# Performance work log

Measured on AMD Instinct MI355X. Metric: run time of the kernel, lower is better.

Reference implementation:

```python
import jax, jax.numpy as jnp
import numpy as np

WINDOW_SIZE = 11
SIGMA = 1.5
C1 = 0.01 ** 2
C2 = 0.03 ** 2


def _gaussian_window(window_size: int, channel: int) -> jnp.ndarray:
    # 1D gaussian, normalized
    g = jnp.arange(window_size, dtype=jnp.float32) - window_size // 2
    g = jnp.exp(-(g ** 2) / (2.0 * SIGMA ** 2))
    g = g / g.sum()
    w2d = jnp.outer(g, g)  # [K, K]
    # depthwise conv kernel: [C, 1, K, K] in OIHW with feature_group_count=C
    return jnp.broadcast_to(w2d[None, None], (channel, 1, window_size, window_size))


def _depthwise_conv(x: jnp.ndarray, window: jnp.ndarray, channel: int) -> jnp.ndarray:
    pad = WINDOW_SIZE // 2
    return jax.lax.conv_general_dilated(
        x, window,
        window_strides=(1, 1),
        padding=((pad, pad), (pad, pad)),
        dimension_numbers=('NCHW', 'OIHW', 'NCHW'),
        feature_group_count=channel,
    )


def setup_inputs() -> dict:
    key = jax.random.key(0)
    k1, k2 = jax.random.split(key)
    shape = (16, 3, 512, 512)
    img1 = jax.random.uniform(k1, shape, dtype=jnp.float32)
    img2 = jax.random.uniform(k2, shape, dtype=jnp.float32)
    return {"img1": img1, "img2": img2}


def reference(img1, img2):
    channel = img1.shape[1]
    window = _gaussian_window(WINDOW_SIZE, channel).astype(img1.dtype)

    mu1 = _depthwise_conv(img1, window, channel)
    mu2 = _depthwise_conv(img2, window, channel)

    mu1_sq = mu1 * mu1
    mu2_sq = mu2 * mu2
    mu1_mu2 = mu1 * mu2

    sigma1_sq = _depthwise_conv(img1 * img1, window, channel) - mu1_sq
    sigma2_sq = _depthwise_conv(img2 * img2, window, channel) - mu2_sq
    sigma12 = _depthwise_conv(img1 * img2, window, channel) - mu1_mu2

    ssim_map = ((2.0 * mu1_mu2 + C1) * (2.0 * sigma12 + C2)) / (
        (mu1_sq + mu2_sq + C1) * (sigma1_sq + sigma2_sq + C2))

    return 1.0 - ssim_map.mean()
```

## Files before the change

### kernel.cpp

```cpp
#include <hip/hip_runtime.h>

#define IMG_W 512
#define IMG_H 512
#define PLANE_PX (IMG_W * IMG_H)
#define N_ELEMS (48 * PLANE_PX)
#define NTHREADS 256
#define TILEW 48
#define NCT 11
#define NBANDS 8
#define NBLK (48 * NBANDS * NCT)

#define C1x2 2.0e-4f
#define C2x2 1.8e-3f

typedef _Float16 h2 __attribute__((ext_vector_type(2)));
typedef _Float16 h8 __attribute__((ext_vector_type(8)));
typedef float f32x4 __attribute__((ext_vector_type(4)));
typedef __fp16 fp16v2 __attribute__((ext_vector_type(2)));

__device__ __forceinline__ h2 h2fma(_Float16 w, h2 v, h2 acc) {
    h2 wv = {w, w};
    return __builtin_elementwise_fma(wv, v, acc);
}
__device__ __forceinline__ unsigned int h2bits(h2 v) {
    union { h2 h; unsigned int u; } c; c.h = v; return c.u;
}
__device__ __forceinline__ h2 pkrtz(float x, float y) {
    union { fp16v2 f; h2 h; } c;
    c.f = __builtin_amdgcn_cvt_pkrtz(x, y);
    return c.h;
}

__global__ void __launch_bounds__(NTHREADS, 5) ssim_main(
    const float* __restrict__ img1, const float* __restrict__ img2,
    float* __restrict__ partials)
{
    __shared__ __align__(16) uint2 R[64 * 64];

    constexpr _Float16 Gh[11] = {
        (_Float16)0.00102838f, (_Float16)0.00759876f, (_Float16)0.03600077f,
        (_Float16)0.10936070f, (_Float16)0.21300553f, (_Float16)0.26601173f,
        (_Float16)0.21300553f, (_Float16)0.10936070f, (_Float16)0.03600077f,
        (_Float16)0.00759876f, (_Float16)0.00102838f
    };

    const int tid = threadIdx.x;

    const int xcd = blockIdx.x & 7;
    const int idx = blockIdx.x >> 3;
    const int plane = xcd * 6 + idx / 88;
    const int t = idx % 88;
    const int band = t / 11;
    const int ct = t - band * 11;
    const int tx0 = ct * TILEW;
    const int ty0 = band * 64;
    const float* pa = img1 + (size_t)plane * PLANE_PX;
    const float* pb = img2 + (size_t)plane * PLANE_PX;

    const int c = tid & 63;
    const int g = tid >> 6;
    const int gx = tx0 - 5 + c;
    const int cgx = min(max(gx, 0), IMG_W - 1);
    const int ry0 = ty0 + g * 16 - 5;

    float av[26], bv[26];
    const bool intY = (ry0 >= 0) && (ry0 + 26 <= IMG_H);
    if (intY) {
        const float* qa = pa + (size_t)ry0 * IMG_W + cgx;
        const float* qb = pb + (size_t)ry0 * IMG_W + cgx;
#pragma unroll
        for (int j = 0; j < 26; ++j) {
            av[j] = qa[j * IMG_W];
            bv[j] = qb[j * IMG_W];
        }
    } else {
#pragma unroll
        for (int j = 0; j < 26; ++j) {
            int ry = ry0 + j;
            int ryc = min(max(ry, 0), IMG_H - 1);
            float rm = ((unsigned)ry < (unsigned)IMG_H) ? 1.f : 0.f;
            av[j] = pa[(size_t)ryc * IMG_W + cgx] * rm;
            bv[j] = pb[(size_t)ryc * IMG_W + cgx] * rm;
        }
    }

    h2 asd[16], asq[16];
#pragma unroll
    for (int k = 0; k < 16; ++k) { asd[k] = (h2)(_Float16)0; asq[k] = (h2)(_Float16)0; }
#pragma unroll
    for (int j = 0; j < 26; ++j) {
        h2 sd = pkrtz(av[j] + bv[j], av[j] - bv[j]);
        h2 sq = sd * sd;
#pragma unroll
        for (int k = 0; k < 16; ++k) {
            int tt = j - k;
            if (tt >= 0 && tt < 11) {
                asd[k] = h2fma(Gh[tt], sd, asd[k]);
                asq[k] = h2fma(Gh[tt], sq, asq[k]);
            }
        }
    }

    if (ct == 0 || ct == NCT - 1) {
        const _Float16 ml = ((unsigned)gx < (unsigned)IMG_W) ? (_Float16)1.f
                                                             : (_Float16)0.f;
        const h2 mlv = {ml, ml};
#pragma unroll
        for (int k = 0; k < 16; ++k) { asd[k] = asd[k] * mlv; asq[k] = asq[k] * mlv; }
    }
#pragma unroll
    for (int kk = 0; kk < 16; ++kk) {
        const int row = g * 16 + kk;
        const int sc = c ^ ((kk & 7) << 1);
        R[row * 64 + sc] = make_uint2(h2bits(asd[kk]), h2bits(asq[kk]));
    }
    __syncthreads();

    const int lane = tid & 63;
    const int nrow = lane & 15;
    const int khi = lane >> 4;
    const int rs = tid >> 6;
    const int row_lds = rs * 16 + nrow;
    const int swz = (nrow & 7) << 1;
    const uint2* Rrow = R + row_lds * 64;

    int sidx = min(lane, 10 - lane);
    unsigned gvb = 0u;
    gvb = (sidx == 0) ? 0x1436u : gvb;
    gvb = (sidx == 1) ? 0x1FC8u : gvb;
    gvb = (sidx == 2) ? 0x289Cu : gvb;
    gvb = (sidx == 3) ? 0x2F00u : gvb;
    gvb = (sidx == 4) ? 0x32D1u : gvb;
    gvb = (sidx == 5) ? 0x3442u : gvb;
    union { h8 h; unsigned u[4]; } af;
#pragma unroll
    for (int w = 0; w < 4; ++w) {
        int t0 = khi * 8 + 2 * w - nrow;
        unsigned lo = (unsigned)__shfl((int)gvb, t0 & 63, 64);
        unsigned hi = (unsigned)__shfl((int)gvb, (t0 + 1) & 63, 64);
        af.u[w] = (lo & 0xFFFFu) | (hi << 16);
    }

    float local = 0.f;
#pragma unroll
    for (int mg = 0; mg < 3; ++mg) {
        if (tx0 + mg * 16 < IMG_W) {
            const int cb = mg * 16 + khi * 8;
            const uint4 q0 = *(const uint4*)&Rrow[(cb + 0) ^ swz];
            const uint4 q1 = *(const uint4*)&Rrow[(cb + 2) ^ swz];
            const uint4 q2 = *(const uint4*)&Rrow[(cb + 4) ^ swz];
            const uint4 q3 = *(const uint4*)&Rrow[(cb + 6) ^ swz];

            union { h8 h; unsigned u[4]; } fs, fd, fss, fdd;
            fs.u[0]  = (q0.x & 0xFFFFu) | (q0.z << 16);
            fs.u[1]  = (q1.x & 0xFFFFu) | (q1.z << 16);
            fs.u[2]  = (q2.x & 0xFFFFu) | (q2.z << 16);
            fs.u[3]  = (q3.x & 0xFFFFu) | (q3.z << 16);
            fd.u[0]  = (q0.x >> 16) | (q0.z & 0xFFFF0000u);
            fd.u[1]  = (q1.x >> 16) | (q1.z & 0xFFFF0000u);
            fd.u[2]  = (q2.x >> 16) | (q2.z & 0xFFFF0000u);
            fd.u[3]  = (q3.x >> 16) | (q3.z & 0xFFFF0000u);
            fss.u[0] = (q0.y & 0xFFFFu) | (q0.w << 16);
            fss.u[1] = (q1.y & 0xFFFFu) | (q1.w << 16);
            fss.u[2] = (q2.y & 0xFFFFu) | (q2.w << 16);
            fss.u[3] = (q3.y & 0xFFFFu) | (q3.w << 16);
            fdd.u[0] = (q0.y >> 16) | (q0.w & 0xFFFF0000u);
            fdd.u[1] = (q1.y >> 16) | (q1.w & 0xFFFF0000u);
            fdd.u[2] = (q2.y >> 16) | (q2.w & 0xFFFF0000u);
            fdd.u[3] = (q3.y >> 16) | (q3.w & 0xFFFF0000u);

            const f32x4 z = {0.f, 0.f, 0.f, 0.f};
            f32x4 aS  = __builtin_amdgcn_mfma_f32_16x16x32_f16(af.h, fs.h,  z, 0, 0, 0);
            f32x4 aD  = __builtin_amdgcn_mfma_f32_16x16x32_f16(af.h, fd.h,  z, 0, 0, 0);
            f32x4 aSS = __builtin_amdgcn_mfma_f32_16x16x32_f16(af.h, fss.h, z, 0, 0, 0);
            f32x4 aDD = __builtin_amdgcn_mfma_f32_16x16x32_f16(af.h, fdd.h, z, 0, 0, 0);

#pragma unroll
            for (int i = 0; i < 4; ++i) {
                float cs = aS[i], cd = aD[i], css = aSS[i], cdd = aDD[i];
                float P = cs * cs, Q = cd * cd;
                float U = P - Q;
                float V = P + Q;
                float num = (U + C1x2) * ((css - cdd) - U + C2x2);
                float den = (V + C1x2) * ((css + cdd) - V + C2x2);
                local += num * __builtin_amdgcn_rcpf(den);
            }
        }
    }

#pragma unroll
    for (int off = 32; off > 0; off >>= 1) local += __shfl_down(local, off, 64);
    __syncthreads();
    float* wp = (float*)R;
    if (lane == 0) wp[rs] = local;
    __syncthreads();
    if (tid == 0)
        partials[blockIdx.x] = wp[0] + wp[1] + wp[2] + wp[3];
}

__global__ void ssim_final(const float* __restrict__ partials,
                           float* __restrict__ out)
{
    __shared__ float wp[4];
    const int tid = threadIdx.x;
    const float4* p4 = (const float4*)partials;
    float s = 0.f;
    for (int i = tid; i < NBLK / 4; i += NTHREADS) {
        float4 v = p4[i];
        s += (v.x + v.y) + (v.z + v.w);
    }
#pragma unroll
    for (int off = 32; off > 0; off >>= 1) s += __shfl_down(s, off, 64);
    if ((tid & 63) == 0) wp[tid >> 6] = s;
    __syncthreads();
    if (tid == 0)
        out[0] = 1.0f - (wp[0] + wp[1] + wp[2] + wp[3]) * (1.0f / (float)N_ELEMS);
}

extern "C" void kernel_launch(void* const* d_in, const int* in_sizes, int n_in,
                              void* d_out, int out_size, void* d_ws, size_t ws_size,
                              hipStream_t stream) {
    const float* img1 = (const float*)d_in[0];
    const float* img2 = (const float*)d_in[1];
    float* out = (float*)d_out;
    float* partials = (float*)d_ws;

    ssim_main<<<NBLK, NTHREADS, 0, stream>>>(img1, img2, partials);
    ssim_final<<<1, NTHREADS, 0, stream>>>(partials, out);
}
```

Before: 127.8 us.

## Move vertical Gaussian pass onto MFMA and store per-quantity planes in LDS

The vertical 11-tap convolution, previously done with scalar packed-half FMAs over 26 register rows per thread, now runs as MFMA 16x16x32 matrix multiplies against a banded Gaussian matrix. Each wave loads 8 rows per lane for 4 column chunks. The results for S, D, SS and DD go into four separate swizzled LDS planes, so the horizontal pass can read each operand with a single 16-byte load and skips the bit-unpacking shuffle. This removes most of the VALU FMA work and the large register arrays, but it adds redundant global loads from overlapping rows and a second fp16 rounding of the intermediate results.

```diff
diff --git a/kernel.cpp b/kernel.cpp
--- a/kernel.cpp
+++ b/kernel.cpp
@@ -18,10 +18,6 @@
 typedef float f32x4 __attribute__((ext_vector_type(4)));
 typedef __fp16 fp16v2 __attribute__((ext_vector_type(2)));
 
-__device__ __forceinline__ h2 h2fma(_Float16 w, h2 v, h2 acc) {
-    h2 wv = {w, w};
-    return __builtin_elementwise_fma(wv, v, acc);
-}
 __device__ __forceinline__ unsigned int h2bits(h2 v) {
     union { h2 h; unsigned int u; } c; c.h = v; return c.u;
 }
@@ -35,94 +31,24 @@
     const float* __restrict__ img1, const float* __restrict__ img2,
     float* __restrict__ partials)
 {
-    __shared__ __align__(16) uint2 R[64 * 64];
-
-    constexpr _Float16 Gh[11] = {
-        (_Float16)0.00102838f, (_Float16)0.00759876f, (_Float16)0.03600077f,
-        (_Float16)0.10936070f, (_Float16)0.21300553f, (_Float16)0.26601173f,
-        (_Float16)0.21300553f, (_Float16)0.10936070f, (_Float16)0.03600077f,
-        (_Float16)0.00759876f, (_Float16)0.00102838f
-    };
+    __shared__ __align__(16) unsigned short P[4 * 64 * 64];
 
     const int tid = threadIdx.x;
+    const int lane = tid & 63;
+    const int wv = tid >> 6;
+    const int nr = lane & 15;
+    const int khi = lane >> 4;
 
     const int xcd = blockIdx.x & 7;
     const int idx = blockIdx.x >> 3;
-    const int plane = xcd * 6 + idx / 88;
+    const int pl = xcd * 6 + idx / 88;
     const int t = idx % 88;
     const int band = t / 11;
     const int ct = t - band * 11;
     const int tx0 = ct * TILEW;
     const int ty0 = band * 64;
-    const float* pa = img1 + (size_t)plane * PLANE_PX;
-    const float* pb = img2 + (size_t)plane * PLANE_PX;
-
-    const int c = tid & 63;
-    const int g = tid >> 6;
-    const int gx = tx0 - 5 + c;
-    const int cgx = min(max(gx, 0), IMG_W - 1);
-    const int ry0 = ty0 + g * 16 - 5;
-
-    float av[26], bv[26];
-    const bool intY = (ry0 >= 0) && (ry0 + 26 <= IMG_H);
-    if (intY) {
-        const float* qa = pa + (size_t)ry0 * IMG_W + cgx;
-        const float* qb = pb + (size_t)ry0 * IMG_W + cgx;
-#pragma unroll
-        for (int j = 0; j < 26; ++j) {
-            av[j] = qa[j * IMG_W];
-            bv[j] = qb[j * IMG_W];
-        }
-    } else {
-#pragma unroll
-        for (int j = 0; j < 26; ++j) {
-            int ry = ry0 + j;
-            int ryc = min(max(ry, 0), IMG_H - 1);
-            float rm = ((unsigned)ry < (unsigned)IMG_H) ? 1.f : 0.f;
-            av[j] = pa[(size_t)ryc * IMG_W + cgx] * rm;
-            bv[j] = pb[(size_t)ryc * IMG_W + cgx] * rm;
-        }
-    }
-
-    h2 asd[16], asq[16];
-#pragma unroll
-    for (int k = 0; k < 16; ++k) { asd[k] = (h2)(_Float16)0; asq[k] = (h2)(_Float16)0; }
-#pragma unroll
-    for (int j = 0; j < 26; ++j) {
-        h2 sd = pkrtz(av[j] + bv[j], av[j] - bv[j]);
-        h2 sq = sd * sd;
-#pragma unroll
-        for (int k = 0; k < 16; ++k) {
-            int tt = j - k;
-            if (tt >= 0 && tt < 11) {
-                asd[k] = h2fma(Gh[tt], sd, asd[k]);
-                asq[k] = h2fma(Gh[tt], sq, asq[k]);
-            }
-        }
-    }
-
-    if (ct == 0 || ct == NCT - 1) {
-        const _Float16 ml = ((unsigned)gx < (unsigned)IMG_W) ? (_Float16)1.f
-                                                             : (_Float16)0.f;
-        const h2 mlv = {ml, ml};
-#pragma unroll
-        for (int k = 0; k < 16; ++k) { asd[k] = asd[k] * mlv; asq[k] = asq[k] * mlv; }
-    }
-#pragma unroll
-    for (int kk = 0; kk < 16; ++kk) {
-        const int row = g * 16 + kk;
-        const int sc = c ^ ((kk & 7) << 1);
-        R[row * 64 + sc] = make_uint2(h2bits(asd[kk]), h2bits(asq[kk]));
-    }
-    __syncthreads();
-
-    const int lane = tid & 63;
-    const int nrow = lane & 15;
-    const int khi = lane >> 4;
-    const int rs = tid >> 6;
-    const int row_lds = rs * 16 + nrow;
-    const int swz = (nrow & 7) << 1;
-    const uint2* Rrow = R + row_lds * 64;
+    const float* pa = img1 + (size_t)pl * PLANE_PX;
+    const float* pb = img2 + (size_t)pl * PLANE_PX;
 
     int sidx = min(lane, 10 - lane);
     unsigned gvb = 0u;
@@ -135,52 +61,102 @@
     union { h8 h; unsigned u[4]; } af;
 #pragma unroll
     for (int w = 0; w < 4; ++w) {
-        int t0 = khi * 8 + 2 * w - nrow;
+        int t0 = khi * 8 + 2 * w - nr;
         unsigned lo = (unsigned)__shfl((int)gvb, t0 & 63, 64);
         unsigned hi = (unsigned)__shfl((int)gvb, (t0 + 1) & 63, 64);
         af.u[w] = (lo & 0xFFFFu) | (hi << 16);
     }
 
+    const f32x4 z = {0.f, 0.f, 0.f, 0.f};
+
+    const int ry0 = ty0 + wv * 16 - 5;
+    const int ryb = ry0 + khi * 8;
+    const bool fastY = (ry0 >= 0) && (ry0 + 31 < IMG_H);
+    const bool edge = (ct == 0) || (ct == NCT - 1);
+
+#pragma unroll
+    for (int tc = 0; tc < 4; ++tc) {
+        const int gx = tx0 - 5 + tc * 16 + nr;
+        const int cgx = min(max(gx, 0), IMG_W - 1);
+        float s[8], d[8];
+        if (fastY) {
+            const float* qa = pa + (size_t)ryb * IMG_W + cgx;
+            const float* qb = pb + (size_t)ryb * IMG_W + cgx;
+#pragma unroll
+            for (int j = 0; j < 8; ++j) {
+                float a = qa[j * IMG_W], b = qb[j * IMG_W];
+                s[j] = a + b; d[j] = a - b;
+            }
+        } else {
+#pragma unroll
+            for (int j = 0; j < 8; ++j) {
+                int ry = ryb + j;
+                int ryc = min(max(ry, 0), IMG_H - 1);
+                float rm = ((unsigned)ry < (unsigned)IMG_H) ? 1.f : 0.f;
+                float a = pa[(size_t)ryc * IMG_W + cgx] * rm;
+                float b = pb[(size_t)ryc * IMG_W + cgx] * rm;
+                s[j] = a + b; d[j] = a - b;
+            }
+        }
+        union { h8 h; h2 p[4]; } FS, FD, FSS, FDD;
+#pragma unroll
+        for (int w = 0; w < 4; ++w) {
+            FS.p[w] = pkrtz(s[2 * w], s[2 * w + 1]);
+            FD.p[w] = pkrtz(d[2 * w], d[2 * w + 1]);
+        }
+        if (edge) {
+            const _Float16 ml = ((unsigned)gx < (unsigned)IMG_W) ? (_Float16)1.f
+                                                                 : (_Float16)0.f;
+            const h2 mlv = {ml, ml};
+#pragma unroll
+            for (int w = 0; w < 4; ++w) { FS.p[w] *= mlv; FD.p[w] *= mlv; }
+        }
+#pragma unroll
+        for (int w = 0; w < 4; ++w) {
+            FSS.p[w] = FS.p[w] * FS.p[w];
+            FDD.p[w] = FD.p[w] * FD.p[w];
+        }
+        f32x4 oS  = __builtin_amdgcn_mfma_f32_16x16x32_f16(FS.h,  af.h, z, 0, 0, 0);
+        f32x4 oD  = __builtin_amdgcn_mfma_f32_16x16x32_f16(FD.h,  af.h, z, 0, 0, 0);
+        f32x4 oSS = __builtin_amdgcn_mfma_f32_16x16x32_f16(FSS.h, af.h, z, 0, 0, 0);
+        f32x4 oDD = __builtin_amdgcn_mfma_f32_16x16x32_f16(FDD.h, af.h, z, 0, 0, 0);
+
+        const int prow = wv * 16 + nr;
+        const int swc = (tc * 16 + khi * 4) ^ ((nr & 7) << 3);
+        unsigned short* q = &P[prow * 64 + swc];
+        *(uint2*)(q)         = make_uint2(h2bits(pkrtz(oS[0],  oS[1])),
+                                          h2bits(pkrtz(oS[2],  oS[3])));
+        *(uint2*)(q + 4096)  = make_uint2(h2bits(pkrtz(oD[0],  oD[1])),
+                                          h2bits(pkrtz(oD[2],  oD[3])));
+        *(uint2*)(q + 8192)  = make_uint2(h2bits(pkrtz(oSS[0], oSS[1])),
+                                          h2bits(pkrtz(oSS[2], oSS[3])));
+        *(uint2*)(q + 12288) = make_uint2(h2bits(pkrtz(oDD[0], oDD[1])),
+                                          h2bits(pkrtz(oDD[2], oDD[3])));
+    }
+    __syncthreads();
+
+    const int row = wv * 16 + nr;
     float local = 0.f;
 #pragma unroll
     for (int mg = 0; mg < 3; ++mg) {
         if (tx0 + mg * 16 < IMG_W) {
-            const int cb = mg * 16 + khi * 8;
-            const uint4 q0 = *(const uint4*)&Rrow[(cb + 0) ^ swz];
-            const uint4 q1 = *(const uint4*)&Rrow[(cb + 2) ^ swz];
-            const uint4 q2 = *(const uint4*)&Rrow[(cb + 4) ^ swz];
-            const uint4 q3 = *(const uint4*)&Rrow[(cb + 6) ^ swz];
-
-            union { h8 h; unsigned u[4]; } fs, fd, fss, fdd;
-            fs.u[0]  = (q0.x & 0xFFFFu) | (q0.z << 16);
-            fs.u[1]  = (q1.x & 0xFFFFu) | (q1.z << 16);
-            fs.u[2]  = (q2.x & 0xFFFFu) | (q2.z << 16);
-            fs.u[3]  = (q3.x & 0xFFFFu) | (q3.z << 16);
-            fd.u[0]  = (q0.x >> 16) | (q0.z & 0xFFFF0000u);
-            fd.u[1]  = (q1.x >> 16) | (q1.z & 0xFFFF0000u);
-            fd.u[2]  = (q2.x >> 16) | (q2.z & 0xFFFF0000u);
-            fd.u[3]  = (q3.x >> 16) | (q3.z & 0xFFFF0000u);
-            fss.u[0] = (q0.y & 0xFFFFu) | (q0.w << 16);
-            fss.u[1] = (q1.y & 0xFFFFu) | (q1.w << 16);
-            fss.u[2] = (q2.y & 0xFFFFu) | (q2.w << 16);
-            fss.u[3] = (q3.y & 0xFFFFu) | (q3.w << 16);
-            fdd.u[0] = (q0.y >> 16) | (q0.w & 0xFFFF0000u);
-            fdd.u[1] = (q1.y >> 16) | (q1.w & 0xFFFF0000u);
-            fdd.u[2] = (q2.y >> 16) | (q2.w & 0xFFFF0000u);
-            fdd.u[3] = (q3.y >> 16) | (q3.w & 0xFFFF0000u);
-
-            const f32x4 z = {0.f, 0.f, 0.f, 0.f};
-            f32x4 aS  = __builtin_amdgcn_mfma_f32_16x16x32_f16(af.h, fs.h,  z, 0, 0, 0);
-            f32x4 aD  = __builtin_amdgcn_mfma_f32_16x16x32_f16(af.h, fd.h,  z, 0, 0, 0);
-            f32x4 aSS = __builtin_amdgcn_mfma_f32_16x16x32_f16(af.h, fss.h, z, 0, 0, 0);
-            f32x4 aDD = __builtin_amdgcn_mfma_f32_16x16x32_f16(af.h, fdd.h, z, 0, 0, 0);
+            const int gi = ((mg * 2 + khi) ^ (nr & 7)) * 8;
+            const unsigned short* base = &P[row * 64 + gi];
+            h8 fS  = *(const h8*)(base);
+            h8 fD  = *(const h8*)(base + 4096);
+            h8 fSS = *(const h8*)(base + 8192);
+            h8 fDD = *(const h8*)(base + 12288);
+            f32x4 aS  = __builtin_amdgcn_mfma_f32_16x16x32_f16(af.h, fS,  z, 0, 0, 0);
+            f32x4 aD  = __builtin_amdgcn_mfma_f32_16x16x32_f16(af.h, fD,  z, 0, 0, 0);
+            f32x4 aSS = __builtin_amdgcn_mfma_f32_16x16x32_f16(af.h, fSS, z, 0, 0, 0);
+            f32x4 aDD = __builtin_amdgcn_mfma_f32_16x16x32_f16(af.h, fDD, z, 0, 0, 0);
 
 #pragma unroll
             for (int i = 0; i < 4; ++i) {
                 float cs = aS[i], cd = aD[i], css = aSS[i], cdd = aDD[i];
-                float P = cs * cs, Q = cd * cd;
-                float U = P - Q;
-                float V = P + Q;
+                float Pq = cs * cs, Qq = cd * cd;
+                float U = Pq - Qq;
+                float V = Pq + Qq;
                 float num = (U + C1x2) * ((css - cdd) - U + C2x2);
                 float den = (V + C1x2) * ((css + cdd) - V + C2x2);
                 local += num * __builtin_amdgcn_rcpf(den);
@@ -191,8 +167,8 @@
 #pragma unroll
     for (int off = 32; off > 0; off >>= 1) local += __shfl_down(local, off, 64);
     __syncthreads();
-    float* wp = (float*)R;
-    if (lane == 0) wp[rs] = local;
+    float* wp = (float*)P;
+    if (lane == 0) wp[wv] = local;
     __syncthreads();
     if (tid == 0)
         partials[blockIdx.x] = wp[0] + wp[1] + wp[2] + wp[3];
```

New measurement: 134.7 us. 1.05x slower.

## Halve row-band height and split MFMA column groups across wave pairs

Applied to the files above, without the earlier changes.

Shrinks each block's tile from 64 to 32 output rows, doubling the grid. Each wave now loads 18 input rows instead of 26 and keeps 8 vertical accumulators instead of 16. Launch bounds rise to 8 blocks per CU and the LDS buffer is halved, aiming at higher occupancy and shorter per-block latency. The horizontal MFMA pass now splits the three 16-column groups between two waves sharing a row set, which leaves the wave pair with uneven work. The taller relative halo also adds redundant loads and vertical FMAs per output.

```diff
diff --git a/kernel.cpp b/kernel.cpp
--- a/kernel.cpp
+++ b/kernel.cpp
@@ -7,7 +7,7 @@
 #define NTHREADS 256
 #define TILEW 48
 #define NCT 11
-#define NBANDS 8
+#define NBANDS 16
 #define NBLK (48 * NBANDS * NCT)
 
 #define C1x2 2.0e-4f
@@ -31,11 +31,11 @@
     return c.h;
 }
 
-__global__ void __launch_bounds__(NTHREADS, 5) ssim_main(
+__global__ void __launch_bounds__(NTHREADS, 8) ssim_main(
     const float* __restrict__ img1, const float* __restrict__ img2,
     float* __restrict__ partials)
 {
-    __shared__ __align__(16) uint2 R[64 * 64];
+    __shared__ __align__(16) uint2 R[32 * 64];
 
     constexpr _Float16 Gh[11] = {
         (_Float16)0.00102838f, (_Float16)0.00759876f, (_Float16)0.03600077f,
@@ -45,37 +45,39 @@
     };
 
     const int tid = threadIdx.x;
+    const int lane = tid & 63;
+    const int wv = tid >> 6;
 
     const int xcd = blockIdx.x & 7;
     const int idx = blockIdx.x >> 3;
-    const int plane = xcd * 6 + idx / 88;
-    const int t = idx % 88;
+    const int pl = xcd * 6 + idx / 176;
+    const int t = idx % 176;
     const int band = t / 11;
     const int ct = t - band * 11;
     const int tx0 = ct * TILEW;
-    const int ty0 = band * 64;
-    const float* pa = img1 + (size_t)plane * PLANE_PX;
-    const float* pb = img2 + (size_t)plane * PLANE_PX;
-
-    const int c = tid & 63;
-    const int g = tid >> 6;
+    const int ty0 = band * 32;
+    const float* pa = img1 + (size_t)pl * PLANE_PX;
+    const float* pb = img2 + (size_t)pl * PLANE_PX;
+
+    const int c = lane;
+    const int g = wv;
     const int gx = tx0 - 5 + c;
     const int cgx = min(max(gx, 0), IMG_W - 1);
-    const int ry0 = ty0 + g * 16 - 5;
-
-    float av[26], bv[26];
-    const bool intY = (ry0 >= 0) && (ry0 + 26 <= IMG_H);
+    const int ry0 = ty0 + g * 8 - 5;
+
+    float av[18], bv[18];
+    const bool intY = (ry0 >= 0) && (ry0 + 18 <= IMG_H);
     if (intY) {
         const float* qa = pa + (size_t)ry0 * IMG_W + cgx;
         const float* qb = pb + (size_t)ry0 * IMG_W + cgx;
 #pragma unroll
-        for (int j = 0; j < 26; ++j) {
+        for (int j = 0; j < 18; ++j) {
             av[j] = qa[j * IMG_W];
             bv[j] = qb[j * IMG_W];
         }
     } else {
 #pragma unroll
-        for (int j = 0; j < 26; ++j) {
+        for (int j = 0; j < 18; ++j) {
             int ry = ry0 + j;
             int ryc = min(max(ry, 0), IMG_H - 1);
             float rm = ((unsigned)ry < (unsigned)IMG_H) ? 1.f : 0.f;
@@ -84,15 +86,15 @@
         }
     }
 
-    h2 asd[16], asq[16];
-#pragma unroll
-    for (int k = 0; k < 16; ++k) { asd[k] = (h2)(_Float16)0; asq[k] = (h2)(_Float16)0; }
-#pragma unroll
-    for (int j = 0; j < 26; ++j) {
+    h2 asd[8], asq[8];
+#pragma unroll
+    for (int k = 0; k < 8; ++k) { asd[k] = (h2)(_Float16)0; asq[k] = (h2)(_Float16)0; }
+#pragma unroll
+    for (int j = 0; j < 18; ++j) {
         h2 sd = pkrtz(av[j] + bv[j], av[j] - bv[j]);
         h2 sq = sd * sd;
 #pragma unroll
-        for (int k = 0; k < 16; ++k) {
+        for (int k = 0; k < 8; ++k) {
             int tt = j - k;
             if (tt >= 0 && tt < 11) {
                 asd[k] = h2fma(Gh[tt], sd, asd[k]);
@@ -106,21 +108,20 @@
                                                              : (_Float16)0.f;
         const h2 mlv = {ml, ml};
 #pragma unroll
-        for (int k = 0; k < 16; ++k) { asd[k] = asd[k] * mlv; asq[k] = asq[k] * mlv; }
-    }
-#pragma unroll
-    for (int kk = 0; kk < 16; ++kk) {
-        const int row = g * 16 + kk;
-        const int sc = c ^ ((kk & 7) << 1);
-        R[row * 64 + sc] = make_uint2(h2bits(asd[kk]), h2bits(asq[kk]));
-    }
-    __syncthreads();
-
-    const int lane = tid & 63;
+        for (int k = 0; k < 8; ++k) { asd[k] = asd[k] * mlv; asq[k] = asq[k] * mlv; }
+    }
+#pragma unroll
+    for (int k = 0; k < 8; ++k) {
+        const int row = g * 8 + k;
+        const int sc = c ^ ((k & 7) << 1);
+        R[row * 64 + sc] = make_uint2(h2bits(asd[k]), h2bits(asq[k]));
+    }
+    __syncthreads();
+
     const int nrow = lane & 15;
     const int khi = lane >> 4;
-    const int rs = tid >> 6;
-    const int row_lds = rs * 16 + nrow;
+    const int rset = wv >> 1;
+    const int row_lds = rset * 16 + nrow;
     const int swz = (nrow & 7) << 1;
     const uint2* Rrow = R + row_lds * 64;
 
@@ -141,10 +142,11 @@
         af.u[w] = (lo & 0xFFFFu) | (hi << 16);
     }
 
+    const f32x4 z = {0.f, 0.f, 0.f, 0.f};
     float local = 0.f;
 #pragma unroll
     for (int mg = 0; mg < 3; ++mg) {
-        if (tx0 + mg * 16 < IMG_W) {
+        if (((mg >> 1) == (wv & 1)) && (tx0 + mg * 16 < IMG_W)) {
             const int cb = mg * 16 + khi * 8;
             const uint4 q0 = *(const uint4*)&Rrow[(cb + 0) ^ swz];
             const uint4 q1 = *(const uint4*)&Rrow[(cb + 2) ^ swz];
@@ -169,7 +171,6 @@
             fdd.u[2] = (q2.y >> 16) | (q2.w & 0xFFFF0000u);
             fdd.u[3] = (q3.y >> 16) | (q3.w & 0xFFFF0000u);
 
-            const f32x4 z = {0.f, 0.f, 0.f, 0.f};
             f32x4 aS  = __builtin_amdgcn_mfma_f32_16x16x32_f16(af.h, fs.h,  z, 0, 0, 0);
             f32x4 aD  = __builtin_amdgcn_mfma_f32_16x16x32_f16(af.h, fd.h,  z, 0, 0, 0);
             f32x4 aSS = __builtin_amdgcn_mfma_f32_16x16x32_f16(af.h, fss.h, z, 0, 0, 0);
@@ -178,9 +179,9 @@
 #pragma unroll
             for (int i = 0; i < 4; ++i) {
                 float cs = aS[i], cd = aD[i], css = aSS[i], cdd = aDD[i];
-                float P = cs * cs, Q = cd * cd;
-                float U = P - Q;
-                float V = P + Q;
+                float Pq = cs * cs, Qq = cd * cd;
+                float U = Pq - Qq;
+                float V = Pq + Qq;
                 float num = (U + C1x2) * ((css - cdd) - U + C2x2);
                 float den = (V + C1x2) * ((css + cdd) - V + C2x2);
                 local += num * __builtin_amdgcn_rcpf(den);
@@ -192,7 +193,7 @@
     for (int off = 32; off > 0; off >>= 1) local += __shfl_down(local, off, 64);
     __syncthreads();
     float* wp = (float*)R;
-    if (lane == 0) wp[rs] = local;
+    if (lane == 0) wp[wv] = local;
     __syncthreads();
     if (tid == 0)
         partials[blockIdx.x] = wp[0] + wp[1] + wp[2] + wp[3];
```

Result: slower. 133.8 us (+4.7%).

## Retile to full-width 16-row bands to remove horizontal halo redundancy

Applied to the files above, without the earlier changes.

Each block now covers a full 512-column by 16-row strip of one plane with 512 threads, in place of 48x64 tiles with a 64-column halo. Horizontal zero padding is written as explicit zero columns in LDS, so no column clamping or masking is needed, and each wave runs four MFMA horizontal passes. This removes the redundant horizontal halo loads and vertical-pass compute (64 columns loaded per 48 outputs). In exchange, the vertical halo grows relative to output: 26 rows loaded for 16 output rows instead of 26 for 16 per thread group, same ratio, and there are fewer, larger blocks.

```diff
diff --git a/kernel.cpp b/kernel.cpp
--- a/kernel.cpp
+++ b/kernel.cpp
@@ -4,11 +4,10 @@
 #define IMG_H 512
 #define PLANE_PX (IMG_W * IMG_H)
 #define N_ELEMS (48 * PLANE_PX)
-#define NTHREADS 256
-#define TILEW 48
-#define NCT 11
-#define NBANDS 8
-#define NBLK (48 * NBANDS * NCT)
+#define NT_MAIN 512
+#define NBANDS 32
+#define NBLK (48 * NBANDS)
+#define RSTR 528
 
 #define C1x2 2.0e-4f
 #define C2x2 1.8e-3f
@@ -31,11 +30,11 @@
     return c.h;
 }
 
-__global__ void __launch_bounds__(NTHREADS, 5) ssim_main(
+__global__ void __launch_bounds__(NT_MAIN, 4) ssim_main(
     const float* __restrict__ img1, const float* __restrict__ img2,
     float* __restrict__ partials)
 {
-    __shared__ __align__(16) uint2 R[64 * 64];
+    __shared__ __align__(16) uint2 R[16 * RSTR];
 
     constexpr _Float16 Gh[11] = {
         (_Float16)0.00102838f, (_Float16)0.00759876f, (_Float16)0.03600077f,
@@ -45,29 +44,34 @@
     };
 
     const int tid = threadIdx.x;
+    const int lane = tid & 63;
+    const int wv = tid >> 6;
 
     const int xcd = blockIdx.x & 7;
     const int idx = blockIdx.x >> 3;
-    const int plane = xcd * 6 + idx / 88;
-    const int t = idx % 88;
-    const int band = t / 11;
-    const int ct = t - band * 11;
-    const int tx0 = ct * TILEW;
-    const int ty0 = band * 64;
-    const float* pa = img1 + (size_t)plane * PLANE_PX;
-    const float* pb = img2 + (size_t)plane * PLANE_PX;
-
-    const int c = tid & 63;
-    const int g = tid >> 6;
-    const int gx = tx0 - 5 + c;
-    const int cgx = min(max(gx, 0), IMG_W - 1);
-    const int ry0 = ty0 + g * 16 - 5;
-
+    const int pl = xcd * 6 + idx / NBANDS;
+    const int band = idx & (NBANDS - 1);
+    const int ty0 = band * 16;
+    const float* pa = img1 + (size_t)pl * PLANE_PX;
+    const float* pb = img2 + (size_t)pl * PLANE_PX;
+
+    if (tid < 16) {
+        const int s = (tid & 7) << 1;
+        uint2* row = R + tid * RSTR;
+#pragma unroll
+        for (int k = 0; k < 8; ++k) {
+            row[k ^ s] = make_uint2(0u, 0u);
+            row[(520 + k) ^ s] = make_uint2(0u, 0u);
+        }
+    }
+
+    const int c = tid;
+    const int ry0 = ty0 - 5;
     float av[26], bv[26];
     const bool intY = (ry0 >= 0) && (ry0 + 26 <= IMG_H);
     if (intY) {
-        const float* qa = pa + (size_t)ry0 * IMG_W + cgx;
-        const float* qb = pb + (size_t)ry0 * IMG_W + cgx;
+        const float* qa = pa + (size_t)ry0 * IMG_W + c;
+        const float* qb = pb + (size_t)ry0 * IMG_W + c;
 #pragma unroll
         for (int j = 0; j < 26; ++j) {
             av[j] = qa[j * IMG_W];
@@ -79,8 +83,8 @@
             int ry = ry0 + j;
             int ryc = min(max(ry, 0), IMG_H - 1);
             float rm = ((unsigned)ry < (unsigned)IMG_H) ? 1.f : 0.f;
-            av[j] = pa[(size_t)ryc * IMG_W + cgx] * rm;
-            bv[j] = pb[(size_t)ryc * IMG_W + cgx] * rm;
+            av[j] = pa[(size_t)ryc * IMG_W + c] * rm;
+            bv[j] = pb[(size_t)ryc * IMG_W + c] * rm;
         }
     }
 
@@ -100,29 +104,17 @@
             }
         }
     }
-
-    if (ct == 0 || ct == NCT - 1) {
-        const _Float16 ml = ((unsigned)gx < (unsigned)IMG_W) ? (_Float16)1.f
-                                                             : (_Float16)0.f;
-        const h2 mlv = {ml, ml};
-#pragma unroll
-        for (int k = 0; k < 16; ++k) { asd[k] = asd[k] * mlv; asq[k] = asq[k] * mlv; }
-    }
-#pragma unroll
-    for (int kk = 0; kk < 16; ++kk) {
-        const int row = g * 16 + kk;
-        const int sc = c ^ ((kk & 7) << 1);
-        R[row * 64 + sc] = make_uint2(h2bits(asd[kk]), h2bits(asq[kk]));
-    }
-    __syncthreads();
-
-    const int lane = tid & 63;
+#pragma unroll
+    for (int k = 0; k < 16; ++k) {
+        const int sc = (8 + c) ^ ((k & 7) << 1);
+        R[k * RSTR + sc] = make_uint2(h2bits(asd[k]), h2bits(asq[k]));
+    }
+    __syncthreads();
+
     const int nrow = lane & 15;
     const int khi = lane >> 4;
-    const int rs = tid >> 6;
-    const int row_lds = rs * 16 + nrow;
     const int swz = (nrow & 7) << 1;
-    const uint2* Rrow = R + row_lds * 64;
+    const uint2* Rrow = R + nrow * RSTR;
 
     int sidx = min(lane, 10 - lane);
     unsigned gvb = 0u;
@@ -136,55 +128,54 @@
 #pragma unroll
     for (int w = 0; w < 4; ++w) {
         int t0 = khi * 8 + 2 * w - nrow;
-        unsigned lo = (unsigned)__shfl((int)gvb, t0 & 63, 64);
-        unsigned hi = (unsigned)__shfl((int)gvb, (t0 + 1) & 63, 64);
+        unsigned lo = (unsigned)__shfl((int)gvb, (t0 - 3) & 63, 64);
+        unsigned hi = (unsigned)__shfl((int)gvb, (t0 - 2) & 63, 64);
         af.u[w] = (lo & 0xFFFFu) | (hi << 16);
     }
 
+    const f32x4 z = {0.f, 0.f, 0.f, 0.f};
     float local = 0.f;
 #pragma unroll
-    for (int mg = 0; mg < 3; ++mg) {
-        if (tx0 + mg * 16 < IMG_W) {
-            const int cb = mg * 16 + khi * 8;
-            const uint4 q0 = *(const uint4*)&Rrow[(cb + 0) ^ swz];
-            const uint4 q1 = *(const uint4*)&Rrow[(cb + 2) ^ swz];
-            const uint4 q2 = *(const uint4*)&Rrow[(cb + 4) ^ swz];
-            const uint4 q3 = *(const uint4*)&Rrow[(cb + 6) ^ swz];
-
-            union { h8 h; unsigned u[4]; } fs, fd, fss, fdd;
-            fs.u[0]  = (q0.x & 0xFFFFu) | (q0.z << 16);
-            fs.u[1]  = (q1.x & 0xFFFFu) | (q1.z << 16);
-            fs.u[2]  = (q2.x & 0xFFFFu) | (q2.z << 16);
-            fs.u[3]  = (q3.x & 0xFFFFu) | (q3.z << 16);
-            fd.u[0]  = (q0.x >> 16) | (q0.z & 0xFFFF0000u);
-            fd.u[1]  = (q1.x >> 16) | (q1.z & 0xFFFF0000u);
-            fd.u[2]  = (q2.x >> 16) | (q2.z & 0xFFFF0000u);
-            fd.u[3]  = (q3.x >> 16) | (q3.z & 0xFFFF0000u);
-            fss.u[0] = (q0.y & 0xFFFFu) | (q0.w << 16);
-            fss.u[1] = (q1.y & 0xFFFFu) | (q1.w << 16);
-            fss.u[2] = (q2.y & 0xFFFFu) | (q2.w << 16);
-            fss.u[3] = (q3.y & 0xFFFFu) | (q3.w << 16);
-            fdd.u[0] = (q0.y >> 16) | (q0.w & 0xFFFF0000u);
-            fdd.u[1] = (q1.y >> 16) | (q1.w & 0xFFFF0000u);
-            fdd.u[2] = (q2.y >> 16) | (q2.w & 0xFFFF0000u);
-            fdd.u[3] = (q3.y >> 16) | (q3.w & 0xFFFF0000u);
-
-            const f32x4 z = {0.f, 0.f, 0.f, 0.f};
-            f32x4 aS  = __builtin_amdgcn_mfma_f32_16x16x32_f16(af.h, fs.h,  z, 0, 0, 0);
-            f32x4 aD  = __builtin_amdgcn_mfma_f32_16x16x32_f16(af.h, fd.h,  z, 0, 0, 0);
-            f32x4 aSS = __builtin_amdgcn_mfma_f32_16x16x32_f16(af.h, fss.h, z, 0, 0, 0);
-            f32x4 aDD = __builtin_amdgcn_mfma_f32_16x16x32_f16(af.h, fdd.h, z, 0, 0, 0);
-
-#pragma unroll
-            for (int i = 0; i < 4; ++i) {
-                float cs = aS[i], cd = aD[i], css = aSS[i], cdd = aDD[i];
-                float P = cs * cs, Q = cd * cd;
-                float U = P - Q;
-                float V = P + Q;
-                float num = (U + C1x2) * ((css - cdd) - U + C2x2);
-                float den = (V + C1x2) * ((css + cdd) - V + C2x2);
-                local += num * __builtin_amdgcn_rcpf(den);
-            }
+    for (int ii = 0; ii < 4; ++ii) {
+        const int ox0 = (wv * 4 + ii) * 16;
+        const int cb = ox0 + khi * 8;
+        const uint4 q0 = *(const uint4*)&Rrow[(cb + 0) ^ swz];
+        const uint4 q1 = *(const uint4*)&Rrow[(cb + 2) ^ swz];
+        const uint4 q2 = *(const uint4*)&Rrow[(cb + 4) ^ swz];
+        const uint4 q3 = *(const uint4*)&Rrow[(cb + 6) ^ swz];
+
+        union { h8 h; unsigned u[4]; } fs, fd, fss, fdd;
+        fs.u[0]  = (q0.x & 0xFFFFu) | (q0.z << 16);
+        fs.u[1]  = (q1.x & 0xFFFFu) | (q1.z << 16);
+        fs.u[2]  = (q2.x & 0xFFFFu) | (q2.z << 16);
+        fs.u[3]  = (q3.x & 0xFFFFu) | (q3.z << 16);
+        fd.u[0]  = (q0.x >> 16) | (q0.z & 0xFFFF0000u);
+        fd.u[1]  = (q1.x >> 16) | (q1.z & 0xFFFF0000u);
+        fd.u[2]  = (q2.x >> 16) | (q2.z & 0xFFFF0000u);
+        fd.u[3]  = (q3.x >> 16) | (q3.z & 0xFFFF0000u);
+        fss.u[0] = (q0.y & 0xFFFFu) | (q0.w << 16);
+        fss.u[1] = (q1.y & 0xFFFFu) | (q1.w << 16);
+        fss.u[2] = (q2.y & 0xFFFFu) | (q2.w << 16);
+        fss.u[3] = (q3.y & 0xFFFFu) | (q3.w << 16);
+        fdd.u[0] = (q0.y >> 16) | (q0.w & 0xFFFF0000u);
+        fdd.u[1] = (q1.y >> 16) | (q1.w & 0xFFFF0000u);
+        fdd.u[2] = (q2.y >> 16) | (q2.w & 0xFFFF0000u);
+        fdd.u[3] = (q3.y >> 16) | (q3.w & 0xFFFF0000u);
+
+        f32x4 aS  = __builtin_amdgcn_mfma_f32_16x16x32_f16(af.h, fs.h,  z, 0, 0, 0);
+        f32x4 aD  = __builtin_amdgcn_mfma_f32_16x16x32_f16(af.h, fd.h,  z, 0, 0, 0);
+        f32x4 aSS = __builtin_amdgcn_mfma_f32_16x16x32_f16(af.h, fss.h, z, 0, 0, 0);
+        f32x4 aDD = __builtin_amdgcn_mfma_f32_16x16x32_f16(af.h, fdd.h, z, 0, 0, 0);
+
+#pragma unroll
+        for (int i = 0; i < 4; ++i) {
+            float cs = aS[i], cd = aD[i], css = aSS[i], cdd = aDD[i];
+            float Pq = cs * cs, Qq = cd * cd;
+            float U = Pq - Qq;
+            float V = Pq + Qq;
+            float num = (U + C1x2) * ((css - cdd) - U + C2x2);
+            float den = (V + C1x2) * ((css + cdd) - V + C2x2);
+            local += num * __builtin_amdgcn_rcpf(den);
         }
     }
 
@@ -192,10 +183,14 @@
     for (int off = 32; off > 0; off >>= 1) local += __shfl_down(local, off, 64);
     __syncthreads();
     float* wp = (float*)R;
-    if (lane == 0) wp[rs] = local;
-    __syncthreads();
-    if (tid == 0)
-        partials[blockIdx.x] = wp[0] + wp[1] + wp[2] + wp[3];
+    if (lane == 0) wp[wv] = local;
+    __syncthreads();
+    if (tid == 0) {
+        float s = 0.f;
+#pragma unroll
+        for (int w = 0; w < 8; ++w) s += wp[w];
+        partials[blockIdx.x] = s;
+    }
 }
 
 __global__ void ssim_final(const float* __restrict__ partials,
@@ -205,7 +200,7 @@
     const int tid = threadIdx.x;
     const float4* p4 = (const float4*)partials;
     float s = 0.f;
-    for (int i = tid; i < NBLK / 4; i += NTHREADS) {
+    for (int i = tid; i < NBLK / 4; i += 256) {
         float4 v = p4[i];
         s += (v.x + v.y) + (v.z + v.w);
     }
@@ -225,6 +220,6 @@
     float* out = (float*)d_out;
     float* partials = (float*)d_ws;
 
-    ssim_main<<<NBLK, NTHREADS, 0, stream>>>(img1, img2, partials);
-    ssim_final<<<1, NTHREADS, 0, stream>>>(partials, out);
-}
+    ssim_main<<<NBLK, NT_MAIN, 0, stream>>>(img1, img2, partials);
+    ssim_final<<<1, 256, 0, stream>>>(partials, out);
+}
```

Result: faster. 121.2 us (-5.2%).
